# Optimization experiments

Hardware: AMD Instinct MI355X
Metric: run time of the kernel (lower is better)

## Reference

```python
import jax, jax.numpy as jnp
import numpy as np

N = 50000      # nodes
D = 128        # feature dim
NNZ = 800000   # edges (avg degree 16)
M = 30         # Chebyshev order

def setup_inputs() -> dict:
    key = jax.random.key(0)
    k1, k2, k3, k4, k5 = jax.random.split(key, 5)
    rows = jax.random.randint(k1, (NNZ,), 0, N)
    cols = jax.random.randint(k2, (NNZ,), 0, N)
    # scale so row sums (Gershgorin bound on spectral radius) stay ~< 1,
    # mimicking a rescaled Laplacian required for a stable Chebyshev recurrence
    vals = jax.random.uniform(k3, (NNZ,), dtype=jnp.float32) * (0.5 / 16.0)
    X = jax.random.normal(k4, (N, D), dtype=jnp.float32)
    coeffs = jax.random.normal(k5, (M,), dtype=jnp.float32)
    return {"rows": rows, "cols": cols, "vals": vals, "X": X, "coeffs": coeffs}

def _spmm(rows, cols, vals, X, n):
    # y[r] += vals[e] * X[c]  for each edge e=(r,c): sparse L @ X
    return jax.ops.segment_sum(vals[:, None] * X[cols], rows, num_segments=n)

def reference(rows, cols, vals, X, coeffs):
    n = X.shape[0]
    T0 = X                                   # T_0 = X
    T1 = _spmm(rows, cols, vals, X, n)       # T_1 = L @ X
    acc = coeffs[0] * T0 + coeffs[1] * T1
    def step(carry, ck):
        T0, T1, acc = carry
        Tk = 2.0 * _spmm(rows, cols, vals, T1, n) - T0   # T_k = 2 L T_{k-1} - T_{k-2}
        return (T1, Tk, acc + ck * Tk), None
    (_, _, acc), _ = jax.lax.scan(step, (T0, T1, acc), coeffs[2:])
    return acc
```

## Files before the change

### kernel.cpp

```cpp
#include <hip/hip_runtime.h>
#include <hip/hip_fp16.h>

#define FD 128
#define RPB 4


__global__ void zero_i32(int* __restrict__ p, int n) {
  int i = blockIdx.x * blockDim.x + threadIdx.x;
  if (i < n) p[i] = 0;
}

__global__ void hist_kernel(const int* __restrict__ rows, int* __restrict__ cnt, int nnz) {
  int i = blockIdx.x * blockDim.x + threadIdx.x;
  if (i < nnz) atomicAdd(&cnt[rows[i]], 1);
}

__global__ void block_reduce(const int* __restrict__ cnt, int* __restrict__ bsum, int n) {
  __shared__ int sm[256];
  int i = blockIdx.x * 256 + threadIdx.x;
  sm[threadIdx.x] = (i < n) ? cnt[i] : 0;
  __syncthreads();
  for (int off = 128; off > 0; off >>= 1) {
    if (threadIdx.x < off) sm[threadIdx.x] += sm[threadIdx.x + off];
    __syncthreads();
  }
  if (threadIdx.x == 0) bsum[blockIdx.x] = sm[0];
}

__global__ void scan_bsum(const int* __restrict__ bsum, int* __restrict__ bpre, int nb) {
  __shared__ int sm[1024];
  const int tid = threadIdx.x;
  sm[tid] = (tid < nb) ? bsum[tid] : 0;
  __syncthreads();
  for (int off = 1; off < 1024; off <<= 1) {
    int t = (tid >= off) ? sm[tid - off] : 0;
    __syncthreads();
    sm[tid] += t;
    __syncthreads();
  }
  if (tid < nb) bpre[tid] = (tid == 0) ? 0 : sm[tid - 1];
}

__global__ void block_scan(const int* __restrict__ cnt, const int* __restrict__ bpre,
                           int* __restrict__ row_ptr, int n) {
  __shared__ int sm[256];
  const int tid = threadIdx.x;
  int i = blockIdx.x * 256 + tid;
  sm[tid] = (i < n) ? cnt[i] : 0;
  __syncthreads();
  for (int off = 1; off < 256; off <<= 1) {
    int t = (tid >= off) ? sm[tid - off] : 0;
    __syncthreads();
    sm[tid] += t;
    __syncthreads();
  }
  if (i < n) row_ptr[i + 1] = sm[tid] + bpre[blockIdx.x];
  if (i == 0) row_ptr[0] = 0;
}

__global__ void copy_i32(const int* __restrict__ src, int* __restrict__ dst, int n) {
  int i = blockIdx.x * blockDim.x + threadIdx.x;
  if (i < n) dst[i] = src[i];
}

__global__ void scatter_kernel(const int* __restrict__ rows, const int* __restrict__ cols,
                               const float* __restrict__ vals, int* __restrict__ fill,
                               int2* __restrict__ pk, int nnz) {
  int i = blockIdx.x * blockDim.x + threadIdx.x;
  if (i < nnz) {
    int r = rows[i];
    int pos = atomicAdd(&fill[r], 1);
    pk[pos] = make_int2(cols[i] << 8, __float_as_int(vals[i]));
  }
}

__global__ void f32_to_f16(const float* __restrict__ src, __half* __restrict__ dst, int n4) {
  int i = blockIdx.x * blockDim.x + threadIdx.x;
  if (i < n4) {
    float4 v = ((const float4*)src)[i];
    __half2* d = (__half2*)dst + 2 * (size_t)i;
    d[0] = __floats2half2_rn(v.x, v.y);
    d[1] = __floats2half2_rn(v.z, v.w);
  }
}


__device__ __forceinline__ void fma_edge(const char* __restrict__ Tfl, int cb, float v,
                                         float2 acc[4]) {
  uint4 raw = *(const uint4*)(Tfl + cb);
  const __half2* h = (const __half2*)&raw;
  float2 x0 = __half22float2(h[0]);
  float2 x1 = __half22float2(h[1]);
  float2 x2 = __half22float2(h[2]);
  float2 x3 = __half22float2(h[3]);
  acc[0].x = fmaf(v, x0.x, acc[0].x); acc[0].y = fmaf(v, x0.y, acc[0].y);
  acc[1].x = fmaf(v, x1.x, acc[1].x); acc[1].y = fmaf(v, x1.y, acc[1].y);
  acc[2].x = fmaf(v, x2.x, acc[2].x); acc[2].y = fmaf(v, x2.y, acc[2].y);
  acc[3].x = fmaf(v, x3.x, acc[3].x); acc[3].y = fmaf(v, x3.y, acc[3].y);
}

__device__ __forceinline__ void gather_row(const int* __restrict__ rp,
                                           const int2* __restrict__ pk,
                                           const char* __restrict__ Tfl,
                                           int r, int sub, float2 acc[4]) {
  int e = rp[r];
  const int end = rp[r + 1];
  for (; e + 16 <= end; e += 16) {
    int2 cv0 = pk[e + sub];
    int2 cv1 = pk[e + 4 + sub];
    int2 cv2 = pk[e + 8 + sub];
    int2 cv3 = pk[e + 12 + sub];
    fma_edge(Tfl, cv0.x, __int_as_float(cv0.y), acc);
    fma_edge(Tfl, cv1.x, __int_as_float(cv1.y), acc);
    fma_edge(Tfl, cv2.x, __int_as_float(cv2.y), acc);
    fma_edge(Tfl, cv3.x, __int_as_float(cv3.y), acc);
  }
  if (e + 8 <= end) {
    int2 cv0 = pk[e + sub];
    int2 cv1 = pk[e + 4 + sub];
    fma_edge(Tfl, cv0.x, __int_as_float(cv0.y), acc);
    fma_edge(Tfl, cv1.x, __int_as_float(cv1.y), acc);
    e += 8;
  }
  if (e + 4 <= end) {
    int2 cv = pk[e + sub];
    fma_edge(Tfl, cv.x, __int_as_float(cv.y), acc);
    e += 4;
  }
  if (e < end) {
    int idx = e + sub;
    int2 cv = pk[min(idx, end - 1)];
    float v = (idx < end) ? __int_as_float(cv.y) : 0.f;
    fma_edge(Tfl, cv.x, v, acc);
  }
}

__device__ __forceinline__ void reduce_subs(float2 acc[4]) {
#pragma unroll
  for (int m = 16; m < 64; m <<= 1) {
#pragma unroll
    for (int q = 0; q < 4; ++q) {
      acc[q].x += __shfl_xor(acc[q].x, m, 64);
      acc[q].y += __shfl_xor(acc[q].y, m, 64);
    }
  }
}


__global__ __launch_bounds__(256) void clen_step(
    const int* __restrict__ rp, const int2* __restrict__ pk,
    const __half* __restrict__ src, const __half* __restrict__ Xh, __half* pd,
    const float* __restrict__ coeffs, int k, int flags, int M, int n) {
  const int lane = threadIdx.x & 63;
  const int sub = lane >> 4, fl = lane & 15;
  const int r = blockIdx.x * RPB + (threadIdx.x >> 6);
  if (r >= n) return;
  const char* Tfl = (const char*)src + fl * 16;

  uint4 xr = make_uint4(0, 0, 0, 0);
  uint4 prr = make_uint4(0, 0, 0, 0);
  if (sub == 0) {
    xr = ((const uint4*)(Xh + (size_t)r * FD))[fl];
    if (flags & 1) prr = ((const uint4*)(pd + (size_t)r * FD))[fl];
  }

  float2 acc[4] = {{0.f,0.f},{0.f,0.f},{0.f,0.f},{0.f,0.f}};
  gather_row(rp, pk, Tfl, r, sub, acc);
  reduce_subs(acc);

  if (sub == 0) {
    float ck = coeffs[k];
    if (flags & 2) ck -= coeffs[M - 1];
    const float g2 = (flags & 4) ? 2.f * coeffs[M - 1] : 2.f;
    const __half2* xh = (const __half2*)&xr;
    float2 p[4] = {{0.f,0.f},{0.f,0.f},{0.f,0.f},{0.f,0.f}};
    if (flags & 1) {
      const __half2* ph = (const __half2*)&prr;
#pragma unroll
      for (int q = 0; q < 4; ++q) p[q] = __half22float2(ph[q]);
    }
    uint4 orr;
    __half2* oh = (__half2*)&orr;
#pragma unroll
    for (int q = 0; q < 4; ++q) {
      float2 x = __half22float2(xh[q]);
      float tx = fmaf(g2, acc[q].x, fmaf(ck, x.x, -p[q].x));
      float ty = fmaf(g2, acc[q].y, fmaf(ck, x.y, -p[q].y));
      oh[q] = __floats2half2_rn(tx, ty);
    }
    ((uint4*)(pd + (size_t)r * FD))[fl] = orr;
  }
}

__global__ __launch_bounds__(256) void clen_final(
    const int* __restrict__ rp, const int2* __restrict__ pk,
    const __half* __restrict__ b1, const __half* __restrict__ b2,
    const float* __restrict__ X, float* __restrict__ out,
    const float* __restrict__ coeffs, int n) {
  const int lane = threadIdx.x & 63;
  const int sub = lane >> 4, fl = lane & 15;
  const int r = blockIdx.x * RPB + (threadIdx.x >> 6);
  if (r >= n) return;
  const char* Tfl = (const char*)b1 + fl * 16;

  uint4 prr = make_uint4(0, 0, 0, 0);
  float4 x0 = make_float4(0.f, 0.f, 0.f, 0.f);
  float4 x1 = make_float4(0.f, 0.f, 0.f, 0.f);
  if (sub == 0) {
    prr = ((const uint4*)(b2 + (size_t)r * FD))[fl];
    x0 = ((const float4*)(X + (size_t)r * FD))[fl * 2];
    x1 = ((const float4*)(X + (size_t)r * FD))[fl * 2 + 1];
  }

  float2 acc[4] = {{0.f,0.f},{0.f,0.f},{0.f,0.f},{0.f,0.f}};
  gather_row(rp, pk, Tfl, r, sub, acc);
  reduce_subs(acc);

  if (sub == 0) {
    const float c0 = coeffs[0];
    const __half2* ph = (const __half2*)&prr;
    float2 p0 = __half22float2(ph[0]), p1 = __half22float2(ph[1]);
    float2 p2 = __half22float2(ph[2]), p3 = __half22float2(ph[3]);
    float4 o0, o1;
    o0.x = fmaf(c0, x0.x, acc[0].x - p0.x);
    o0.y = fmaf(c0, x0.y, acc[0].y - p0.y);
    o0.z = fmaf(c0, x0.z, acc[1].x - p1.x);
    o0.w = fmaf(c0, x0.w, acc[1].y - p1.y);
    o1.x = fmaf(c0, x1.x, acc[2].x - p2.x);
    o1.y = fmaf(c0, x1.y, acc[2].y - p2.y);
    o1.z = fmaf(c0, x1.z, acc[3].x - p3.x);
    o1.w = fmaf(c0, x1.w, acc[3].y - p3.y);
    ((float4*)(out + (size_t)r * FD))[fl * 2] = o0;
    ((float4*)(out + (size_t)r * FD))[fl * 2 + 1] = o1;
  }
}


extern "C" void kernel_launch(void* const* d_in, const int* in_sizes, int n_in,
                              void* d_out, int out_size, void* d_ws, size_t ws_size,
                              hipStream_t stream) {
  const int* rows = (const int*)d_in[0];
  const int* cols = (const int*)d_in[1];
  const float* vals = (const float*)d_in[2];
  const float* X = (const float*)d_in[3];
  const float* coeffs = (const float*)d_in[4];
  float* out = (float*)d_out;

  const int nnz = in_sizes[0];
  const int n = in_sizes[3] / FD;
  const int M = in_sizes[4];

  auto align_up = [](size_t x) { return (x + 255) & ~(size_t)255; };
  char* w = (char*)d_ws;
  size_t off = 0;
  int* row_ptr = (int*)(w + off); off = align_up(off + (size_t)(n + 1) * 4);
  int* row_fill = (int*)(w + off); off = align_up(off + (size_t)n * 4);
  int* bsum = (int*)(w + off); off = align_up(off + 1024 * 4);
  int* bpre = (int*)(w + off); off = align_up(off + 1024 * 4);
  int2* pk = (int2*)(w + off); off = align_up(off + (size_t)nnz * 8);
  __half* Xh = (__half*)(w + off); off = align_up(off + (size_t)n * FD * 2);
  __half* buf0 = (__half*)(w + off); off = align_up(off + (size_t)n * FD * 2);
  __half* buf1 = (__half*)(w + off); off = align_up(off + (size_t)n * FD * 2);
  __half* bufs[2] = {buf0, buf1};
  (void)ws_size;

  const int B = 256;
  const int gN = (n + B - 1) / B;
  const int gE = (nnz + B - 1) / B;
  const int gS = (n + RPB - 1) / RPB;
  const int n4 = n * FD / 4;
  const int gC = (n4 + B - 1) / B;

  zero_i32<<<gN, B, 0, stream>>>(row_fill, n);
  hist_kernel<<<gE, B, 0, stream>>>(rows, row_fill, nnz);
  block_reduce<<<gN, B, 0, stream>>>(row_fill, bsum, n);
  scan_bsum<<<1, 1024, 0, stream>>>(bsum, bpre, gN);
  block_scan<<<gN, B, 0, stream>>>(row_fill, bpre, row_ptr, n);
  copy_i32<<<gN, B, 0, stream>>>(row_ptr, row_fill, n);
  scatter_kernel<<<gE, B, 0, stream>>>(rows, cols, vals, row_fill, pk, nnz);
  f32_to_f16<<<gC, B, 0, stream>>>(X, Xh, n4);

  clen_step<<<gS, B, 0, stream>>>(row_ptr, pk, Xh, Xh, bufs[(M - 2) & 1],
                                  coeffs, M - 2, 4, M, n);
  clen_step<<<gS, B, 0, stream>>>(row_ptr, pk, bufs[(M - 2) & 1], Xh, bufs[(M - 3) & 1],
                                  coeffs, M - 3, 2, M, n);
  for (int k = M - 4; k >= 1; --k) {
    clen_step<<<gS, B, 0, stream>>>(row_ptr, pk, bufs[(k + 1) & 1], Xh, bufs[k & 1],
                                    coeffs, k, 1, M, n);
  }
  clen_final<<<gS, B, 0, stream>>>(row_ptr, pk, bufs[1], bufs[0], X, out, coeffs, n);
}
```

Baseline: 1.129 ms.

## Gather FP8 copies of recurrence vectors in SpMM, keep FP16 for recurrence terms

Each Clenshaw step now also writes an FP8 (e4m3) copy of its output, and the sparse gather in the next step reads that FP8 copy instead of the FP16 buffer. This halves the bytes fetched per gathered neighbour row. The lane mapping changes from 4 edge groups by 16 feature lanes to 8 edge groups by 8 lanes, each lane holding 16 accumulators, and the cross-lane reduction gains one more shuffle stage. The cost is much lower precision in the gathered operand, which can build up over 30 recurrence steps, plus an extra FP8 write per step.

New measurement: 1.338 ms. +18.5%, slower.

```diff
diff --git a/kernel.cpp b/kernel.cpp
--- a/kernel.cpp
+++ b/kernel.cpp
@@ -70,101 +70,109 @@
   if (i < nnz) {
     int r = rows[i];
     int pos = atomicAdd(&fill[r], 1);
-    pk[pos] = make_int2(cols[i] << 8, __float_as_int(vals[i]));
-  }
-}
-
-__global__ void f32_to_f16(const float* __restrict__ src, __half* __restrict__ dst, int n4) {
+    pk[pos] = make_int2(cols[i] << 7, __float_as_int(vals[i]));
+  }
+}
+
+__global__ void f32_to_f16_f8(const float* __restrict__ src, __half* __restrict__ dst,
+                              unsigned int* __restrict__ dst8, int n4) {
   int i = blockIdx.x * blockDim.x + threadIdx.x;
   if (i < n4) {
     float4 v = ((const float4*)src)[i];
     __half2* d = (__half2*)dst + 2 * (size_t)i;
     d[0] = __floats2half2_rn(v.x, v.y);
     d[1] = __floats2half2_rn(v.z, v.w);
-  }
-}
-
-
-__device__ __forceinline__ void fma_edge(const char* __restrict__ Tfl, int cb, float v,
-                                         float2 acc[4]) {
+    int w = 0;
+    w = __builtin_amdgcn_cvt_pk_fp8_f32(v.x, v.y, w, false);
+    w = __builtin_amdgcn_cvt_pk_fp8_f32(v.z, v.w, w, true);
+    dst8[i] = (unsigned int)w;
+  }
+}
+
+
+typedef float v2f __attribute__((ext_vector_type(2)));
+
+__device__ __forceinline__ void fma_edge8(const char* __restrict__ Tfl, int cb, float v,
+                                          float acc[16]) {
   uint4 raw = *(const uint4*)(Tfl + cb);
-  const __half2* h = (const __half2*)&raw;
-  float2 x0 = __half22float2(h[0]);
-  float2 x1 = __half22float2(h[1]);
-  float2 x2 = __half22float2(h[2]);
-  float2 x3 = __half22float2(h[3]);
-  acc[0].x = fmaf(v, x0.x, acc[0].x); acc[0].y = fmaf(v, x0.y, acc[0].y);
-  acc[1].x = fmaf(v, x1.x, acc[1].x); acc[1].y = fmaf(v, x1.y, acc[1].y);
-  acc[2].x = fmaf(v, x2.x, acc[2].x); acc[2].y = fmaf(v, x2.y, acc[2].y);
-  acc[3].x = fmaf(v, x3.x, acc[3].x); acc[3].y = fmaf(v, x3.y, acc[3].y);
+  v2f f;
+  f = __builtin_amdgcn_cvt_pk_f32_fp8((int)raw.x, false);
+  acc[0] = fmaf(v, f.x, acc[0]);  acc[1] = fmaf(v, f.y, acc[1]);
+  f = __builtin_amdgcn_cvt_pk_f32_fp8((int)raw.x, true);
+  acc[2] = fmaf(v, f.x, acc[2]);  acc[3] = fmaf(v, f.y, acc[3]);
+  f = __builtin_amdgcn_cvt_pk_f32_fp8((int)raw.y, false);
+  acc[4] = fmaf(v, f.x, acc[4]);  acc[5] = fmaf(v, f.y, acc[5]);
+  f = __builtin_amdgcn_cvt_pk_f32_fp8((int)raw.y, true);
+  acc[6] = fmaf(v, f.x, acc[6]);  acc[7] = fmaf(v, f.y, acc[7]);
+  f = __builtin_amdgcn_cvt_pk_f32_fp8((int)raw.z, false);
+  acc[8] = fmaf(v, f.x, acc[8]);  acc[9] = fmaf(v, f.y, acc[9]);
+  f = __builtin_amdgcn_cvt_pk_f32_fp8((int)raw.z, true);
+  acc[10] = fmaf(v, f.x, acc[10]); acc[11] = fmaf(v, f.y, acc[11]);
+  f = __builtin_amdgcn_cvt_pk_f32_fp8((int)raw.w, false);
+  acc[12] = fmaf(v, f.x, acc[12]); acc[13] = fmaf(v, f.y, acc[13]);
+  f = __builtin_amdgcn_cvt_pk_f32_fp8((int)raw.w, true);
+  acc[14] = fmaf(v, f.x, acc[14]); acc[15] = fmaf(v, f.y, acc[15]);
 }
 
 __device__ __forceinline__ void gather_row(const int* __restrict__ rp,
                                            const int2* __restrict__ pk,
                                            const char* __restrict__ Tfl,
-                                           int r, int sub, float2 acc[4]) {
+                                           int r, int sub, float acc[16]) {
   int e = rp[r];
   const int end = rp[r + 1];
   for (; e + 16 <= end; e += 16) {
     int2 cv0 = pk[e + sub];
-    int2 cv1 = pk[e + 4 + sub];
-    int2 cv2 = pk[e + 8 + sub];
-    int2 cv3 = pk[e + 12 + sub];
-    fma_edge(Tfl, cv0.x, __int_as_float(cv0.y), acc);
-    fma_edge(Tfl, cv1.x, __int_as_float(cv1.y), acc);
-    fma_edge(Tfl, cv2.x, __int_as_float(cv2.y), acc);
-    fma_edge(Tfl, cv3.x, __int_as_float(cv3.y), acc);
+    int2 cv1 = pk[e + 8 + sub];
+    fma_edge8(Tfl, cv0.x, __int_as_float(cv0.y), acc);
+    fma_edge8(Tfl, cv1.x, __int_as_float(cv1.y), acc);
   }
   if (e + 8 <= end) {
-    int2 cv0 = pk[e + sub];
-    int2 cv1 = pk[e + 4 + sub];
-    fma_edge(Tfl, cv0.x, __int_as_float(cv0.y), acc);
-    fma_edge(Tfl, cv1.x, __int_as_float(cv1.y), acc);
+    int2 cv = pk[e + sub];
+    fma_edge8(Tfl, cv.x, __int_as_float(cv.y), acc);
     e += 8;
-  }
-  if (e + 4 <= end) {
-    int2 cv = pk[e + sub];
-    fma_edge(Tfl, cv.x, __int_as_float(cv.y), acc);
-    e += 4;
   }
   if (e < end) {
     int idx = e + sub;
     int2 cv = pk[min(idx, end - 1)];
     float v = (idx < end) ? __int_as_float(cv.y) : 0.f;
-    fma_edge(Tfl, cv.x, v, acc);
-  }
-}
-
-__device__ __forceinline__ void reduce_subs(float2 acc[4]) {
-#pragma unroll
-  for (int m = 16; m < 64; m <<= 1) {
-#pragma unroll
-    for (int q = 0; q < 4; ++q) {
-      acc[q].x += __shfl_xor(acc[q].x, m, 64);
-      acc[q].y += __shfl_xor(acc[q].y, m, 64);
-    }
+    fma_edge8(Tfl, cv.x, v, acc);
+  }
+}
+
+__device__ __forceinline__ void reduce_subs(float acc[16]) {
+#pragma unroll
+  for (int m = 8; m < 64; m <<= 1) {
+#pragma unroll
+    for (int j = 0; j < 16; ++j) acc[j] += __shfl_xor(acc[j], m, 64);
   }
 }
 
 
 __global__ __launch_bounds__(256) void clen_step(
     const int* __restrict__ rp, const int2* __restrict__ pk,
-    const __half* __restrict__ src, const __half* __restrict__ Xh, __half* pd,
+    const unsigned char* __restrict__ src8, const __half* __restrict__ Xh, __half* pd,
+    unsigned char* __restrict__ dst8,
     const float* __restrict__ coeffs, int k, int flags, int M, int n) {
   const int lane = threadIdx.x & 63;
-  const int sub = lane >> 4, fl = lane & 15;
+  const int sub = lane >> 3, fl = lane & 7;
   const int r = blockIdx.x * RPB + (threadIdx.x >> 6);
   if (r >= n) return;
-  const char* Tfl = (const char*)src + fl * 16;
-
-  uint4 xr = make_uint4(0, 0, 0, 0);
-  uint4 prr = make_uint4(0, 0, 0, 0);
+  const char* Tfl = (const char*)src8 + fl * 16;
+
+  uint4 xr0 = make_uint4(0,0,0,0), xr1 = make_uint4(0,0,0,0);
+  uint4 pr0 = make_uint4(0,0,0,0), pr1 = make_uint4(0,0,0,0);
   if (sub == 0) {
-    xr = ((const uint4*)(Xh + (size_t)r * FD))[fl];
-    if (flags & 1) prr = ((const uint4*)(pd + (size_t)r * FD))[fl];
-  }
-
-  float2 acc[4] = {{0.f,0.f},{0.f,0.f},{0.f,0.f},{0.f,0.f}};
+    xr0 = ((const uint4*)(Xh + (size_t)r * FD))[fl * 2];
+    xr1 = ((const uint4*)(Xh + (size_t)r * FD))[fl * 2 + 1];
+    if (flags & 1) {
+      pr0 = ((const uint4*)(pd + (size_t)r * FD))[fl * 2];
+      pr1 = ((const uint4*)(pd + (size_t)r * FD))[fl * 2 + 1];
+    }
+  }
+
+  float acc[16];
+#pragma unroll
+  for (int j = 0; j < 16; ++j) acc[j] = 0.f;
   gather_row(rp, pk, Tfl, r, sub, acc);
   reduce_subs(acc);
 
@@ -172,66 +180,115 @@
     float ck = coeffs[k];
     if (flags & 2) ck -= coeffs[M - 1];
     const float g2 = (flags & 4) ? 2.f * coeffs[M - 1] : 2.f;
-    const __half2* xh = (const __half2*)&xr;
-    float2 p[4] = {{0.f,0.f},{0.f,0.f},{0.f,0.f},{0.f,0.f}};
-    if (flags & 1) {
-      const __half2* ph = (const __half2*)&prr;
-#pragma unroll
-      for (int q = 0; q < 4; ++q) p[q] = __half22float2(ph[q]);
-    }
-    uint4 orr;
-    __half2* oh = (__half2*)&orr;
+    const __half2* xh0 = (const __half2*)&xr0;
+    const __half2* xh1 = (const __half2*)&xr1;
+    const __half2* ph0 = (const __half2*)&pr0;
+    const __half2* ph1 = (const __half2*)&pr1;
+    float t[16];
 #pragma unroll
     for (int q = 0; q < 4; ++q) {
-      float2 x = __half22float2(xh[q]);
-      float tx = fmaf(g2, acc[q].x, fmaf(ck, x.x, -p[q].x));
-      float ty = fmaf(g2, acc[q].y, fmaf(ck, x.y, -p[q].y));
-      oh[q] = __floats2half2_rn(tx, ty);
-    }
-    ((uint4*)(pd + (size_t)r * FD))[fl] = orr;
+      float2 x = __half22float2(xh0[q]);
+      float2 p = (flags & 1) ? __half22float2(ph0[q]) : make_float2(0.f, 0.f);
+      t[2*q]   = fmaf(g2, acc[2*q],   fmaf(ck, x.x, -p.x));
+      t[2*q+1] = fmaf(g2, acc[2*q+1], fmaf(ck, x.y, -p.y));
+    }
+#pragma unroll
+    for (int q = 0; q < 4; ++q) {
+      float2 x = __half22float2(xh1[q]);
+      float2 p = (flags & 1) ? __half22float2(ph1[q]) : make_float2(0.f, 0.f);
+      t[8+2*q]   = fmaf(g2, acc[8+2*q],   fmaf(ck, x.x, -p.x));
+      t[8+2*q+1] = fmaf(g2, acc[8+2*q+1], fmaf(ck, x.y, -p.y));
+    }
+    uint4 o0, o1;
+    __half2* oh0 = (__half2*)&o0;
+    __half2* oh1 = (__half2*)&o1;
+#pragma unroll
+    for (int q = 0; q < 4; ++q) {
+      oh0[q] = __floats2half2_rn(t[2*q], t[2*q+1]);
+      oh1[q] = __floats2half2_rn(t[8+2*q], t[8+2*q+1]);
+    }
+    ((uint4*)(pd + (size_t)r * FD))[fl * 2] = o0;
+    ((uint4*)(pd + (size_t)r * FD))[fl * 2 + 1] = o1;
+    uint4 m8;
+    int w;
+    w = 0;
+    w = __builtin_amdgcn_cvt_pk_fp8_f32(t[0], t[1], w, false);
+    w = __builtin_amdgcn_cvt_pk_fp8_f32(t[2], t[3], w, true);
+    m8.x = (unsigned int)w;
+    w = 0;
+    w = __builtin_amdgcn_cvt_pk_fp8_f32(t[4], t[5], w, false);
+    w = __builtin_amdgcn_cvt_pk_fp8_f32(t[6], t[7], w, true);
+    m8.y = (unsigned int)w;
+    w = 0;
+    w = __builtin_amdgcn_cvt_pk_fp8_f32(t[8], t[9], w, false);
+    w = __builtin_amdgcn_cvt_pk_fp8_f32(t[10], t[11], w, true);
+    m8.z = (unsigned int)w;
+    w = 0;
+    w = __builtin_amdgcn_cvt_pk_fp8_f32(t[12], t[13], w, false);
+    w = __builtin_amdgcn_cvt_pk_fp8_f32(t[14], t[15], w, true);
+    m8.w = (unsigned int)w;
+    ((uint4*)(dst8 + (size_t)r * FD))[fl] = m8;
   }
 }
 
 __global__ __launch_bounds__(256) void clen_final(
     const int* __restrict__ rp, const int2* __restrict__ pk,
-    const __half* __restrict__ b1, const __half* __restrict__ b2,
+    const unsigned char* __restrict__ b18, const __half* __restrict__ b2,
     const float* __restrict__ X, float* __restrict__ out,
     const float* __restrict__ coeffs, int n) {
   const int lane = threadIdx.x & 63;
-  const int sub = lane >> 4, fl = lane & 15;
+  const int sub = lane >> 3, fl = lane & 7;
   const int r = blockIdx.x * RPB + (threadIdx.x >> 6);
   if (r >= n) return;
-  const char* Tfl = (const char*)b1 + fl * 16;
-
-  uint4 prr = make_uint4(0, 0, 0, 0);
-  float4 x0 = make_float4(0.f, 0.f, 0.f, 0.f);
-  float4 x1 = make_float4(0.f, 0.f, 0.f, 0.f);
+  const char* Tfl = (const char*)b18 + fl * 16;
+
+  uint4 pr0 = make_uint4(0,0,0,0), pr1 = make_uint4(0,0,0,0);
+  float4 x0 = make_float4(0.f,0.f,0.f,0.f), x1 = make_float4(0.f,0.f,0.f,0.f);
+  float4 x2 = make_float4(0.f,0.f,0.f,0.f), x3 = make_float4(0.f,0.f,0.f,0.f);
   if (sub == 0) {
-    prr = ((const uint4*)(b2 + (size_t)r * FD))[fl];
-    x0 = ((const float4*)(X + (size_t)r * FD))[fl * 2];
-    x1 = ((const float4*)(X + (size_t)r * FD))[fl * 2 + 1];
-  }
-
-  float2 acc[4] = {{0.f,0.f},{0.f,0.f},{0.f,0.f},{0.f,0.f}};
+    pr0 = ((const uint4*)(b2 + (size_t)r * FD))[fl * 2];
+    pr1 = ((const uint4*)(b2 + (size_t)r * FD))[fl * 2 + 1];
+    const float4* Xr = (const float4*)(X + (size_t)r * FD);
+    x0 = Xr[fl * 4]; x1 = Xr[fl * 4 + 1]; x2 = Xr[fl * 4 + 2]; x3 = Xr[fl * 4 + 3];
+  }
+
+  float acc[16];
+#pragma unroll
+  for (int j = 0; j < 16; ++j) acc[j] = 0.f;
   gather_row(rp, pk, Tfl, r, sub, acc);
   reduce_subs(acc);
 
   if (sub == 0) {
     const float c0 = coeffs[0];
-    const __half2* ph = (const __half2*)&prr;
-    float2 p0 = __half22float2(ph[0]), p1 = __half22float2(ph[1]);
-    float2 p2 = __half22float2(ph[2]), p3 = __half22float2(ph[3]);
-    float4 o0, o1;
-    o0.x = fmaf(c0, x0.x, acc[0].x - p0.x);
-    o0.y = fmaf(c0, x0.y, acc[0].y - p0.y);
-    o0.z = fmaf(c0, x0.z, acc[1].x - p1.x);
-    o0.w = fmaf(c0, x0.w, acc[1].y - p1.y);
-    o1.x = fmaf(c0, x1.x, acc[2].x - p2.x);
-    o1.y = fmaf(c0, x1.y, acc[2].y - p2.y);
-    o1.z = fmaf(c0, x1.z, acc[3].x - p3.x);
-    o1.w = fmaf(c0, x1.w, acc[3].y - p3.y);
-    ((float4*)(out + (size_t)r * FD))[fl * 2] = o0;
-    ((float4*)(out + (size_t)r * FD))[fl * 2 + 1] = o1;
+    const __half2* ph0 = (const __half2*)&pr0;
+    const __half2* ph1 = (const __half2*)&pr1;
+    float p[16];
+#pragma unroll
+    for (int q = 0; q < 4; ++q) {
+      float2 a = __half22float2(ph0[q]);
+      p[2*q] = a.x; p[2*q+1] = a.y;
+      float2 b = __half22float2(ph1[q]);
+      p[8+2*q] = b.x; p[8+2*q+1] = b.y;
+    }
+    float4 o0, o1, o2, o3;
+    o0.x = fmaf(c0, x0.x, acc[0] - p[0]);
+    o0.y = fmaf(c0, x0.y, acc[1] - p[1]);
+    o0.z = fmaf(c0, x0.z, acc[2] - p[2]);
+    o0.w = fmaf(c0, x0.w, acc[3] - p[3]);
+    o1.x = fmaf(c0, x1.x, acc[4] - p[4]);
+    o1.y = fmaf(c0, x1.y, acc[5] - p[5]);
+    o1.z = fmaf(c0, x1.z, acc[6] - p[6]);
+    o1.w = fmaf(c0, x1.w, acc[7] - p[7]);
+    o2.x = fmaf(c0, x2.x, acc[8] - p[8]);
+    o2.y = fmaf(c0, x2.y, acc[9] - p[9]);
+    o2.z = fmaf(c0, x2.z, acc[10] - p[10]);
+    o2.w = fmaf(c0, x2.w, acc[11] - p[11]);
+    o3.x = fmaf(c0, x3.x, acc[12] - p[12]);
+    o3.y = fmaf(c0, x3.y, acc[13] - p[13]);
+    o3.z = fmaf(c0, x3.z, acc[14] - p[14]);
+    o3.w = fmaf(c0, x3.w, acc[15] - p[15]);
+    float4* Or = (float4*)(out + (size_t)r * FD);
+    Or[fl * 4] = o0; Or[fl * 4 + 1] = o1; Or[fl * 4 + 2] = o2; Or[fl * 4 + 3] = o3;
   }
 }
 
@@ -261,7 +318,10 @@
   __half* Xh = (__half*)(w + off); off = align_up(off + (size_t)n * FD * 2);
   __half* buf0 = (__half*)(w + off); off = align_up(off + (size_t)n * FD * 2);
   __half* buf1 = (__half*)(w + off); off = align_up(off + (size_t)n * FD * 2);
+  unsigned char* m80 = (unsigned char*)(w + off); off = align_up(off + (size_t)n * FD);
+  unsigned char* m81 = (unsigned char*)(w + off); off = align_up(off + (size_t)n * FD);
   __half* bufs[2] = {buf0, buf1};
+  unsigned char* m8[2] = {m80, m81};
   (void)ws_size;
 
   const int B = 256;
@@ -278,15 +338,15 @@
   block_scan<<<gN, B, 0, stream>>>(row_fill, bpre, row_ptr, n);
   copy_i32<<<gN, B, 0, stream>>>(row_ptr, row_fill, n);
   scatter_kernel<<<gE, B, 0, stream>>>(rows, cols, vals, row_fill, pk, nnz);
-  f32_to_f16<<<gC, B, 0, stream>>>(X, Xh, n4);
-
-  clen_step<<<gS, B, 0, stream>>>(row_ptr, pk, Xh, Xh, bufs[(M - 2) & 1],
-                                  coeffs, M - 2, 4, M, n);
-  clen_step<<<gS, B, 0, stream>>>(row_ptr, pk, bufs[(M - 2) & 1], Xh, bufs[(M - 3) & 1],
-                                  coeffs, M - 3, 2, M, n);
+  f32_to_f16_f8<<<gC, B, 0, stream>>>(X, Xh, (unsigned int*)m8[(M - 1) & 1], n4);
+
+  clen_step<<<gS, B, 0, stream>>>(row_ptr, pk, m8[(M - 1) & 1], Xh, bufs[(M - 2) & 1],
+                                  m8[(M - 2) & 1], coeffs, M - 2, 4, M, n);
+  clen_step<<<gS, B, 0, stream>>>(row_ptr, pk, m8[(M - 2) & 1], Xh, bufs[(M - 3) & 1],
+                                  m8[(M - 3) & 1], coeffs, M - 3, 2, M, n);
   for (int k = M - 4; k >= 1; --k) {
-    clen_step<<<gS, B, 0, stream>>>(row_ptr, pk, bufs[(k + 1) & 1], Xh, bufs[k & 1],
-                                    coeffs, k, 1, M, n);
-  }
-  clen_final<<<gS, B, 0, stream>>>(row_ptr, pk, bufs[1], bufs[0], X, out, coeffs, n);
-}
+    clen_step<<<gS, B, 0, stream>>>(row_ptr, pk, m8[(k + 1) & 1], Xh, bufs[k & 1],
+                                    m8[k & 1], coeffs, k, 1, M, n);
+  }
+  clen_final<<<gS, B, 0, stream>>>(row_ptr, pk, m8[1], bufs[0], X, out, coeffs, n);
+}
```
